# Performance work log

Measured on AMD Instinct MI355X. Metric: run time of the kernel, lower is better.

The kernel has to match this reference:

```python
import jax, jax.numpy as jnp
import numpy as np

SOS = 0
EOS = 1
NEG = -10000.0
B, S, T = 128, 1024, 128


def setup_inputs() -> dict:
    key = jax.random.key(0)
    k1, k2, k3 = jax.random.split(key, 3)
    emissions = jax.random.normal(k1, (B, S, T), dtype=jnp.float32)
    tags = jax.random.randint(k2, (B, S), 0, T)
    mask = jnp.ones((B, S), dtype=jnp.float32)
    transition = jax.random.uniform(k3, (T, T), minval=-0.1, maxval=0.1, dtype=jnp.float32)
    transition = transition.at[:, SOS].set(NEG).at[EOS, :].set(NEG)
    return {"emissions": emissions, "transition": transition, "mask": mask, "tags": tags}


def _crf_nll(emissions, transition, mask, tags):
    b, s, t = emissions.shape
    barange = jnp.arange(b)

    # ---- gold-path score (vectorized over time) ----
    first_tags = tags[:, 0]
    last_valid_idx = mask.astype(jnp.int32).sum(1) - 1
    last_tags = jnp.take_along_axis(tags, last_valid_idx[:, None], axis=1)[:, 0]

    score = transition[SOS, first_tags] + emissions[:, 0][barange, first_tags]
    e_scores = jnp.take_along_axis(emissions, tags[:, :, None], axis=2)[:, :, 0]  # (B,S)
    t_scores = transition[tags[:, :-1], tags[:, 1:]]                              # (B,S-1)
    score = score + ((e_scores[:, 1:] + t_scores) * mask[:, 1:]).sum(axis=1)
    score = score + transition[last_tags, EOS]

    # ---- log partition via forward algorithm (lax.scan over time) ----
    alphas0 = transition[SOS][None, :] + emissions[:, 0]  # (B,T)

    def step(alphas, inp):
        e_i, m_i = inp  # (B,T), (B,)
        # scores[b, prev, cur] = alphas[b, prev] + transition[prev, cur] + e_i[b, cur]
        scores = alphas[:, :, None] + transition[None, :, :] + e_i[:, None, :]
        new_alphas = jax.scipy.special.logsumexp(scores, axis=1)  # (B,T)
        m = m_i[:, None]
        return m * new_alphas + (1.0 - m) * alphas, None

    em_t = jnp.swapaxes(emissions, 0, 1)[1:]  # (S-1, B, T)
    mk_t = mask.T[1:]                         # (S-1, B)
    alphas, _ = jax.lax.scan(step, alphas0, (em_t, mk_t))

    partition = jax.scipy.special.logsumexp(alphas + transition[:, EOS][None, :], axis=1)  # (B,)
    return -jnp.sum(score - partition)


def reference(emissions, transition, mask, tags):
    return _crf_nll(emissions, transition, mask, tags)
```

## Files before the change

kernel.cpp:

```cpp
#include <hip/hip_runtime.h>
#include <cmath>

#define SOS 0
#define EOS 1
#define Bb 128
#define Ss 1024
#define Tt 128
#define LOG2E 1.4426950408889634f
#define LN2f  0.6931471805599453f

__global__ __launch_bounds__(256) void crf_forward(
    const float* __restrict__ em, const float* __restrict__ trans,
    const float* __restrict__ mask, float* __restrict__ part_out)
{
  __shared__ __align__(16) float s_trans[Tt * Tt];
  __shared__ __align__(16) float s_f[Tt];
  __shared__ __align__(16) float s_part[8][Tt];
  __shared__ __align__(16) float s_em[4][Tt];
  __shared__ __align__(16) float s_mask[Ss];
  __shared__ float s_red[4];

  const int tid = threadIdx.x;
  const int b = blockIdx.x;
  const size_t em_base = (size_t)b * Ss * Tt;

  for (int i = tid; i < Ss; i += 256) s_mask[i] = mask[b * Ss + i];
  #pragma unroll
  for (int it = 0; it < (Tt * Tt) / (256 * 4); ++it) {
    int idx = (it * 256 + tid) * 4;
    *(float4*)&s_trans[idx] = *(const float4*)&trans[idx];
  }
  __syncthreads();

  const int ks = tid >> 5;
  const int js = tid & 31;
  const int k0 = ks * 16, j0 = js * 4;
  float Mreg[16][4];
  #pragma unroll
  for (int kk = 0; kk < 16; ++kk)
    #pragma unroll
    for (int jj = 0; jj < 4; ++jj)
      Mreg[kk][jj] = exp2f(s_trans[(k0 + kk) * Tt + (j0 + jj)] * LOG2E);

  float a2 = -3.0e38f;
  if (tid < Tt) a2 = (s_trans[SOS * Tt + tid] + em[em_base + tid]) * LOG2E;
  float wm = a2;
  #pragma unroll
  for (int o = 32; o > 0; o >>= 1) wm = fmaxf(wm, __shfl_xor(wm, o));
  if ((tid & 63) == 0) s_red[tid >> 6] = wm;
  __syncthreads();
  const float m0 = fmaxf(s_red[0], s_red[1]);
  if (tid < Tt) s_f[tid] = exp2f(a2 - m0);
  float c_scale = m0;

  if (tid >= 128 && tid < 160) {
    int lt = tid - 128;
    #pragma unroll
    for (int r = 1; r <= 3; ++r)
      *(float4*)&s_em[r & 3][lt * 4] =
          *(const float4*)&em[em_base + (size_t)r * Tt + lt * 4];
  }
  __syncthreads();

  for (int i = 1; i < Ss; ++i) {
    float fr[16];
    *(float4*)&fr[0]  = *(float4*)&s_f[k0];
    *(float4*)&fr[4]  = *(float4*)&s_f[k0 + 4];
    *(float4*)&fr[8]  = *(float4*)&s_f[k0 + 8];
    *(float4*)&fr[12] = *(float4*)&s_f[k0 + 12];
    float acc0 = 0.f, acc1 = 0.f, acc2 = 0.f, acc3 = 0.f;
    #pragma unroll
    for (int kk = 0; kk < 16; ++kk) {
      float f = fr[kk];
      acc0 += f * Mreg[kk][0];
      acc1 += f * Mreg[kk][1];
      acc2 += f * Mreg[kk][2];
      acc3 += f * Mreg[kk][3];
    }
    *(float4*)&s_part[ks][j0] = make_float4(acc0, acc1, acc2, acc3);
    __syncthreads();

    if (tid < Tt) {
      const int j = tid;
      float g = ((s_part[0][j] + s_part[1][j]) + (s_part[2][j] + s_part[3][j]))
              + ((s_part[4][j] + s_part[5][j]) + (s_part[6][j] + s_part[7][j]));
      float w = exp2f(s_em[i & 3][j] * LOG2E);
      float fn = g * w;
      float mi = s_mask[i];
      float fold = s_f[j];
      if (mi == 0.0f) fn = fold;

      if ((i & 3) == 0) {
        float M = fmaxf(s_red[0], s_red[1]);
        int e;
        (void)frexpf(M, &e);
        float scl = __int_as_float((127 - e) << 23);
        fn *= scl;
        c_scale += (float)e;
      }
      if ((i & 3) == 3) {
        float v = fn;
        #pragma unroll
        for (int o = 32; o > 0; o >>= 1) v = fmaxf(v, __shfl_xor(v, o));
        if ((tid & 63) == 0) s_red[tid >> 6] = v;
      }
      s_f[j] = fn;
    } else if (tid < 160) {
      int r = i + 3;
      if (r < Ss) {
        int lt = tid - 128;
        *(float4*)&s_em[r & 3][lt * 4] =
            *(const float4*)&em[em_base + (size_t)r * Tt + lt * 4];
      }
    }
    __syncthreads();
  }

  float v = 0.f;
  if (tid < Tt) {
    float tE2 = s_trans[tid * Tt + EOS] * LOG2E;
    v = s_f[tid] * exp2f(tE2);
  }
  #pragma unroll
  for (int o = 32; o > 0; o >>= 1) v += __shfl_xor(v, o);
  if ((tid & 63) == 0) s_red[tid >> 6] = v;
  __syncthreads();
  if (tid == 0) {
    float s = s_red[0] + s_red[1];
    part_out[b] = (log2f(s) + c_scale) * LN2f;
  }
}

__global__ __launch_bounds__(256) void crf_score(
    const float* __restrict__ em, const float* __restrict__ trans,
    const float* __restrict__ mask, const int* __restrict__ tags,
    float* __restrict__ sc)
{
  __shared__ float s_red[4];
  __shared__ float s_red2[4];
  const int tid = threadIdx.x;
  const int b = blockIdx.x;
  const size_t em_base = (size_t)b * Ss * Tt;
  const int* tg = tags + b * Ss;
  const float* mk = mask + b * Ss;

  float part = 0.f, msum = 0.f;
  for (int i = tid; i < Ss; i += 256) {
    float m = mk[i];
    msum += m;
    if (i >= 1) {
      int tc = tg[i], tp = tg[i - 1];
      part += m * (em[em_base + (size_t)i * Tt + tc] + trans[tp * Tt + tc]);
    }
  }
  #pragma unroll
  for (int o = 32; o > 0; o >>= 1) {
    part += __shfl_xor(part, o);
    msum += __shfl_xor(msum, o);
  }
  if ((tid & 63) == 0) { s_red[tid >> 6] = part; s_red2[tid >> 6] = msum; }
  __syncthreads();
  if (tid == 0) {
    float p  = s_red[0] + s_red[1] + s_red[2] + s_red[3];
    float ms = s_red2[0] + s_red2[1] + s_red2[2] + s_red2[3];
    int last = (int)(ms + 0.5f) - 1;
    int t0 = tg[0];
    float s = trans[SOS * Tt + t0] + em[em_base + t0] + p
            + trans[tg[last] * Tt + EOS];
    sc[b] = s;
  }
}

__global__ __launch_bounds__(128) void crf_combine(
    const float* __restrict__ part, const float* __restrict__ sc,
    float* __restrict__ out)
{
  __shared__ float s_red[2];
  const int tid = threadIdx.x;
  float v = part[tid] - sc[tid];
  #pragma unroll
  for (int o = 32; o > 0; o >>= 1) v += __shfl_xor(v, o);
  if ((tid & 63) == 0) s_red[tid >> 6] = v;
  __syncthreads();
  if (tid == 0) out[0] = s_red[0] + s_red[1];
}

extern "C" void kernel_launch(void* const* d_in, const int* in_sizes, int n_in,
                              void* d_out, int out_size, void* d_ws, size_t ws_size,
                              hipStream_t stream)
{
  const float* em    = (const float*)d_in[0];
  const float* trans = (const float*)d_in[1];
  const float* mask  = (const float*)d_in[2];
  const int*   tags  = (const int*)d_in[3];
  float* out = (float*)d_out;
  float* wsf = (float*)d_ws;
  float* part = wsf;
  float* sc   = wsf + 128;

  hipLaunchKernelGGL(crf_forward, dim3(Bb), dim3(256), 0, stream,
                     em, trans, mask, part);
  hipLaunchKernelGGL(crf_score, dim3(Bb), dim3(256), 0, stream,
                     em, trans, mask, tags, sc);
  hipLaunchKernelGGL(crf_combine, dim3(1), dim3(128), 0, stream,
                     part, sc, out);
}
```

Measured before the change: 515.8 us.

## Remap forward recurrence to one barrier per step with in-warp k-reduction

Each column j is now split across two half-warps, each holding 64 k rows of the exponentiated transition in registers, and the halves are combined with a single cross-lane shuffle. This removes the shared-memory partial-sum array and the second __syncthreads per time step. The state is double-buffered in shared memory, emissions are prefetched into registers two steps ahead, and rescaling is folded into the emission weight. Two further changes ride along: every thread now computes the step redundantly instead of only 128 of them, and the score kernel is launched before the forward kernel.

```diff
diff --git a/kernel.cpp b/kernel.cpp
--- a/kernel.cpp
+++ b/kernel.cpp
@@ -14,119 +14,95 @@
     const float* __restrict__ mask, float* __restrict__ part_out)
 {
   __shared__ __align__(16) float s_trans[Tt * Tt];
-  __shared__ __align__(16) float s_f[Tt];
-  __shared__ __align__(16) float s_part[8][Tt];
-  __shared__ __align__(16) float s_em[4][Tt];
+  __shared__ __align__(16) float s_f[2][Tt];
+  __shared__ __align__(16) float s_red[4];
   __shared__ __align__(16) float s_mask[Ss];
-  __shared__ float s_red[4];
 
   const int tid = threadIdx.x;
-  const int b = blockIdx.x;
-  const size_t em_base = (size_t)b * Ss * Tt;
+  const int w   = tid >> 6;
+  const int l   = tid & 63;
+  const int jl  = l & 31;
+  const int j   = w * 32 + jl;
+  const int kh  = l >> 5;
+  const int kbase = kh * 64;
+  const int b   = blockIdx.x;
+  const size_t base = (size_t)b * Ss * Tt;
 
   for (int i = tid; i < Ss; i += 256) s_mask[i] = mask[b * Ss + i];
   #pragma unroll
-  for (int it = 0; it < (Tt * Tt) / (256 * 4); ++it) {
+  for (int it = 0; it < 16; ++it) {
     int idx = (it * 256 + tid) * 4;
     *(float4*)&s_trans[idx] = *(const float4*)&trans[idx];
   }
+  if (tid < 4) s_red[tid] = 0.5f;
   __syncthreads();
 
-  const int ks = tid >> 5;
-  const int js = tid & 31;
-  const int k0 = ks * 16, j0 = js * 4;
-  float Mreg[16][4];
+  float Mreg[64];
   #pragma unroll
-  for (int kk = 0; kk < 16; ++kk)
-    #pragma unroll
-    for (int jj = 0; jj < 4; ++jj)
-      Mreg[kk][jj] = exp2f(s_trans[(k0 + kk) * Tt + (j0 + jj)] * LOG2E);
+  for (int kk = 0; kk < 64; ++kk)
+    Mreg[kk] = exp2f(s_trans[(kbase + kk) * Tt + j] * LOG2E);
+  const float tSOS  = s_trans[SOS * Tt + j];
+  const float tEOS2 = s_trans[j * Tt + EOS] * LOG2E;
 
-  float a2 = -3.0e38f;
-  if (tid < Tt) a2 = (s_trans[SOS * Tt + tid] + em[em_base + tid]) * LOG2E;
-  float wm = a2;
-  #pragma unroll
-  for (int o = 32; o > 0; o >>= 1) wm = fmaxf(wm, __shfl_xor(wm, o));
-  if ((tid & 63) == 0) s_red[tid >> 6] = wm;
-  __syncthreads();
-  const float m0 = fmaxf(s_red[0], s_red[1]);
-  if (tid < Tt) s_f[tid] = exp2f(a2 - m0);
-  float c_scale = m0;
-
-  if (tid >= 128 && tid < 160) {
-    int lt = tid - 128;
-    #pragma unroll
-    for (int r = 1; r <= 3; ++r)
-      *(float4*)&s_em[r & 3][lt * 4] =
-          *(const float4*)&em[em_base + (size_t)r * Tt + lt * 4];
-  }
+  float fn = exp2f((tSOS + em[base + j]) * LOG2E);
+  if (l < 32) s_f[0][j] = fn;
+  float c_scale = 0.f;
+  float em0 = em[base + (size_t)1 * Tt + j];
+  float em1 = em[base + (size_t)2 * Tt + j];
   __syncthreads();
 
   for (int i = 1; i < Ss; ++i) {
-    float fr[16];
-    *(float4*)&fr[0]  = *(float4*)&s_f[k0];
-    *(float4*)&fr[4]  = *(float4*)&s_f[k0 + 4];
-    *(float4*)&fr[8]  = *(float4*)&s_f[k0 + 8];
-    *(float4*)&fr[12] = *(float4*)&s_f[k0 + 12];
+    const int p = i & 1;
+    int ip = (i + 2 < Ss) ? (i + 2) : (Ss - 1);
+    float em2 = em[base + (size_t)ip * Tt + j];
+    float mi = s_mask[i];
+    float fold = s_f[p ^ 1][j];
+
+    float scl = 1.0f;
+    if ((i & 3) == 1) {
+      float4 r4 = *(float4*)&s_red[0];
+      float M = fmaxf(fmaxf(r4.x, r4.y), fmaxf(r4.z, r4.w));
+      int e; (void)frexpf(M, &e);
+      scl = __int_as_float((127 - e) << 23);
+      c_scale += (float)e;
+    }
+    float w_ = exp2f(em0 * LOG2E) * scl;
+
     float acc0 = 0.f, acc1 = 0.f, acc2 = 0.f, acc3 = 0.f;
+    const float4* fsrc = (const float4*)&s_f[p ^ 1][kbase];
     #pragma unroll
-    for (int kk = 0; kk < 16; ++kk) {
-      float f = fr[kk];
-      acc0 += f * Mreg[kk][0];
-      acc1 += f * Mreg[kk][1];
-      acc2 += f * Mreg[kk][2];
-      acc3 += f * Mreg[kk][3];
+    for (int q = 0; q < 16; ++q) {
+      float4 fv = fsrc[q];
+      acc0 = fmaf(fv.x, Mreg[4 * q + 0], acc0);
+      acc1 = fmaf(fv.y, Mreg[4 * q + 1], acc1);
+      acc2 = fmaf(fv.z, Mreg[4 * q + 2], acc2);
+      acc3 = fmaf(fv.w, Mreg[4 * q + 3], acc3);
     }
-    *(float4*)&s_part[ks][j0] = make_float4(acc0, acc1, acc2, acc3);
-    __syncthreads();
+    float g = (acc0 + acc1) + (acc2 + acc3);
+    g += __shfl_xor(g, 32);
 
-    if (tid < Tt) {
-      const int j = tid;
-      float g = ((s_part[0][j] + s_part[1][j]) + (s_part[2][j] + s_part[3][j]))
-              + ((s_part[4][j] + s_part[5][j]) + (s_part[6][j] + s_part[7][j]));
-      float w = exp2f(s_em[i & 3][j] * LOG2E);
-      float fn = g * w;
-      float mi = s_mask[i];
-      float fold = s_f[j];
-      if (mi == 0.0f) fn = fold;
+    float fnew = g * w_;
+    fold *= scl;
+    fn = (mi == 0.f) ? fold : fnew;
+    if (l < 32) s_f[p][j] = fn;
 
-      if ((i & 3) == 0) {
-        float M = fmaxf(s_red[0], s_red[1]);
-        int e;
-        (void)frexpf(M, &e);
-        float scl = __int_as_float((127 - e) << 23);
-        fn *= scl;
-        c_scale += (float)e;
-      }
-      if ((i & 3) == 3) {
-        float v = fn;
-        #pragma unroll
-        for (int o = 32; o > 0; o >>= 1) v = fmaxf(v, __shfl_xor(v, o));
-        if ((tid & 63) == 0) s_red[tid >> 6] = v;
-      }
-      s_f[j] = fn;
-    } else if (tid < 160) {
-      int r = i + 3;
-      if (r < Ss) {
-        int lt = tid - 128;
-        *(float4*)&s_em[r & 3][lt * 4] =
-            *(const float4*)&em[em_base + (size_t)r * Tt + lt * 4];
-      }
+    if ((i & 3) == 0) {
+      float v = fn;
+      #pragma unroll
+      for (int o = 16; o > 0; o >>= 1) v = fmaxf(v, __shfl_xor(v, o));
+      if (l == 0) s_red[w] = v;
     }
+    em0 = em1; em1 = em2;
     __syncthreads();
   }
 
-  float v = 0.f;
-  if (tid < Tt) {
-    float tE2 = s_trans[tid * Tt + EOS] * LOG2E;
-    v = s_f[tid] * exp2f(tE2);
-  }
+  float v = (l < 32) ? fn * exp2f(tEOS2) : 0.f;
   #pragma unroll
   for (int o = 32; o > 0; o >>= 1) v += __shfl_xor(v, o);
-  if ((tid & 63) == 0) s_red[tid >> 6] = v;
+  if (l == 0) s_red[w] = v;
   __syncthreads();
   if (tid == 0) {
-    float s = s_red[0] + s_red[1];
+    float s = (s_red[0] + s_red[1]) + (s_red[2] + s_red[3]);
     part_out[b] = (log2f(s) + c_scale) * LN2f;
   }
 }
@@ -198,10 +174,10 @@
   float* part = wsf;
   float* sc   = wsf + 128;
 
+  hipLaunchKernelGGL(crf_score, dim3(Bb), dim3(256), 0, stream,
+                     em, trans, mask, tags, sc);
   hipLaunchKernelGGL(crf_forward, dim3(Bb), dim3(256), 0, stream,
                      em, trans, mask, part);
-  hipLaunchKernelGGL(crf_score, dim3(Bb), dim3(256), 0, stream,
-                     em, trans, mask, tags, sc);
   hipLaunchKernelGGL(crf_combine, dim3(1), dim3(128), 0, stream,
                      part, sc, out);
 }
```

Result: slower. 543.3 us (+5.3%).
